# Kernel tuning notes

Measured on AMD Instinct MI355X. Metric: run time of the kernel, lower is better.

The kernel has to match this reference:

```python
import jax, jax.numpy as jnp
import numpy as np

# ---- config (matches init_kwargs) ----
M, N, D = 8, 512, 243            # meshes, neurons per mesh, input dim
E_RATIO = 0.8
NE = int(N * E_RATIO)            # 409 excitatory
NI = N - NE                      # 103 inhibitory
TICKS = 16
BATCH = 512
BITS = 4
WSCALE = 8.0
VTH, VRESET = 1.0, 0.0
TAU_E, TAU_I, DT = 2.0, 1.5, 1.0
BETA = 10.0                      # fast-sigmoid surrogate slope
INPUT_SCALE = 1.0


def fake_quant(w):
    """Quantization-aware fake quant with straight-through estimator."""
    step = WSCALE / (2 ** (BITS - 1))          # 1.0 for 4-bit, scale 8
    q = jnp.clip(jnp.round(w / step), -(2 ** (BITS - 1)), 2 ** (BITS - 1) - 1) * step
    return w + jax.lax.stop_gradient(q - w)


@jax.custom_vjp
def spike(u):
    return (u >= 0.0).astype(u.dtype)

def _spike_fwd(u):
    return spike(u), u

def _spike_bwd(u, g):
    # fast-sigmoid surrogate gradient
    return (g * BETA / (1.0 + BETA * jnp.abs(u)) ** 2,)

spike.defvjp(_spike_fwd, _spike_bwd)


def setup_inputs() -> dict:
    key = jax.random.key(0)
    ks = jax.random.split(key, 8)

    def sparse_w(k, shape, density, std, zero_diag=False):
        km, kw = jax.random.split(k)
        mask = (jax.random.uniform(km, shape) < density).astype(jnp.float32)
        if zero_diag:
            mask = mask * (1.0 - jnp.eye(shape[-1], dtype=jnp.float32))
        return jax.random.normal(kw, shape) * std * mask

    x = jax.random.normal(ks[0], (BATCH, D), dtype=jnp.float32)
    W_in = jax.random.normal(ks[1], (M, N, D)) * 0.8      # per-mesh input projection [out,in]
    b_in = jax.random.normal(ks[2], (M, N)) * 0.05
    W_inter = sparse_w(ks[3], (M, N, NE), 0.3, 0.8)        # inter-mesh: E of mesh m -> mesh m+1
    W_EE = sparse_w(ks[4], (M, NE, NE), 0.5, 0.8, True)
    W_EI = sparse_w(ks[5], (M, NI, NE), 0.6, 0.8)
    W_IE = sparse_w(ks[6], (M, NE, NI), 0.8, 0.8)
    W_II = sparse_w(ks[7], (M, NI, NI), 0.7, 0.8, True)
    return dict(x=x, W_in=W_in, b_in=b_in, W_inter=W_inter,
                W_EE=W_EE, W_EI=W_EI, W_IE=W_IE, W_II=W_II)


def reference(x, W_in, b_in, W_inter, W_EE, W_EI, W_IE, W_II):
    B = x.shape[0]
    decay_E = 1.0 - DT / TAU_E
    decay_I = 1.0 - DT / TAU_I

    # quantize weights once (constant across ticks)
    qW_in, qW_inter = fake_quant(W_in), fake_quant(W_inter)
    qW_EE, qW_EI = fake_quant(W_EE), fake_quant(W_EI)
    qW_IE, qW_II = fake_quant(W_IE), fake_quant(W_II)

    # external input projection, same every tick: [M, B, N]
    ext_proj = jnp.einsum('bd,mnd->mbn', x * INPUT_SCALE, qW_in) + b_in[:, None, :]

    def tick(carry, _):
        e, i, vE, vI, acc = carry          # e:[M,B,NE] i:[M,B,NI]
        # inter-mesh: mesh m receives inter_connections[m-1](e_prev[m-1])
        inter = jnp.einsum('mbe,mne->mbn', e, qW_inter)
        ext = ext_proj + jnp.roll(inter, 1, axis=0)
        cE = ext[:, :, :NE] \
            + jnp.einsum('mbe,mfe->mbf', e, qW_EE) \
            + jnp.einsum('mbi,mfi->mbf', i, qW_IE)
        cI = ext[:, :, NE:] \
            + jnp.einsum('mbe,mfe->mbf', e, qW_EI) \
            + jnp.einsum('mbi,mfi->mbf', i, qW_II)
        # LIF: leaky decay + input, threshold, hard reset
        vE = vE * decay_E + cE * DT
        vI = vI * decay_I + cI * DT
        sE = spike(vE - VTH)
        sI = spike(vI - VTH)
        vE = sE * VRESET + (1.0 - sE) * vE
        vI = sI * VRESET + (1.0 - sI) * vI
        acc = acc + jnp.concatenate([sE, sI], axis=-1)
        return (sE, sI, vE, vI, acc), None

    z = jnp.zeros
    carry0 = (z((M, B, NE)), z((M, B, NI)), z((M, B, NE)), z((M, B, NI)), z((M, B, N)))
    (eF, iF, vEF, vIF, acc), _ = jax.lax.scan(tick, carry0, None, length=TICKS)
    # accumulator laid out mesh-major: [B, M*N]
    return jnp.transpose(acc, (1, 0, 2)).reshape(B, M * N)
```

## Files before the change

kernel.cpp:

```cpp
#include <hip/hip_runtime.h>
#include <hip/hip_bf16.h>

#define Mm 8
#define Nn 512
#define NEe 409
#define NIi 103
#define Bb 512
#define Dd 243
#define Tt 16
#define SPB 96
#define WCROW 1152
#define DEC_I 0.33333334f
#define NBLK 256
#define FLAGSTRIDE 16
#define FLAGINTS 8192
#define SPINMAX 1000000L
#define ABROW 176

typedef int v4i __attribute__((ext_vector_type(4)));

__device__ __forceinline__ float quantf(float w) {
    float q = rintf(w);
    return fminf(fmaxf(q, -8.0f), 7.0f);
}

__device__ __forceinline__ v4i unpack16(unsigned int dl, unsigned int dh, bool qhi, int qsh) {
    unsigned int d = qhi ? dh : dl;
    v4i r;
    r[0] = (int)((((d >> qsh) & 0xFu) * 0x00204081u) & 0x01010101u);
    r[1] = (int)((((d >> (qsh + 4)) & 0xFu) * 0x00204081u) & 0x01010101u);
    r[2] = (int)((((d >> (qsh + 8)) & 0xFu) * 0x00204081u) & 0x01010101u);
    r[3] = (int)((((d >> (qsh + 12)) & 0xFu) * 0x00204081u) & 0x01010101u);
    return r;
}

__global__ void k_pack(const float* __restrict__ Wint, const float* __restrict__ WEE,
                       const float* __restrict__ WEI, const float* __restrict__ WIE,
                       const float* __restrict__ WII, signed char* __restrict__ Wc,
                       int* __restrict__ flags) {
    if (blockIdx.x == 0) {
        for (int i = threadIdx.x; i < FLAGINTS; i += 256) flags[i] = 0;
    }
    int q = blockIdx.x * 256 + threadIdx.x;
    if (q >= (Mm * Nn * WCROW) / 4) return;
    int k0 = (q * 4) % WCROW;
    int n  = ((q * 4) / WCROW) & (Nn - 1);
    int m  = (q * 4) / (WCROW * Nn);
    char out4[4];
#pragma unroll
    for (int j = 0; j < 4; ++j) {
        int k = k0 + j;
        float w = 0.0f;
        if (k < 512) {
            if (k < NEe) w = Wint[((((m + 7) & 7) * Nn) + n) * NEe + k];
        } else if (k < 1024) {
            int jj = k - 512;
            if (jj < NEe) w = (n < NEe) ? WEE[((m * NEe) + n) * NEe + jj]
                                        : WEI[((m * NIi) + (n - NEe)) * NEe + jj];
        } else {
            int jj = k - 1049;
            if (jj >= 0 && jj < NIi) w = (n < NEe) ? WIE[((m * NEe) + n) * NIi + jj]
                                        : WII[((m * NIi) + (n - NEe)) * NIi + jj];
        }
        out4[j] = (signed char)(int)quantf(w);
    }
    *(int*)&Wc[q * 4] = *(int*)out4;
}

__global__ void k_ext(const float* __restrict__ x, const float* __restrict__ Win,
                      const float* __restrict__ bin, float* __restrict__ ext) {
    __shared__ float xs[64][68];
    __shared__ float wsm[64][68];
    const int bid = blockIdx.x;
    const int m  = bid >> 6;
    const int bt = (bid >> 3) & 7;
    const int nt = bid & 7;
    const int b0 = bt * 64, n0 = nt * 64;
    const int t = threadIdx.x;
    const int tb4 = (t & 15) * 4;
    const int tn4 = (t >> 4) * 4;
    const int sr = t >> 2;
    const int sc = (t & 3) * 16;
    float c[4][4];
#pragma unroll
    for (int i = 0; i < 4; ++i)
#pragma unroll
        for (int j = 0; j < 4; ++j) c[i][j] = 0.0f;

    for (int d0 = 0; d0 < Dd; d0 += 64) {
#pragma unroll
        for (int j = 0; j < 16; ++j) {
            int d = d0 + sc + j;
            float xv = 0.0f, wv = 0.0f;
            if (d < Dd) {
                xv = x[(b0 + sr) * Dd + d];
                wv = quantf(Win[((m * Nn) + n0 + sr) * Dd + d]);
            }
            xs[sc + j][sr] = xv;
            wsm[sc + j][sr] = wv;
        }
        __syncthreads();
        const int dmax = min(64, Dd - d0);
        for (int d = 0; d < dmax; ++d) {
            float4 av = *(const float4*)&xs[d][tb4];
            float4 wv = *(const float4*)&wsm[d][tn4];
            float a[4] = {av.x, av.y, av.z, av.w};
            float wq[4] = {wv.x, wv.y, wv.z, wv.w};
#pragma unroll
            for (int i = 0; i < 4; ++i)
#pragma unroll
                for (int j = 0; j < 4; ++j)
                    c[i][j] = fmaf(a[i], wq[j], c[i][j]);
        }
        __syncthreads();
    }
#pragma unroll
    for (int i = 0; i < 4; ++i)
#pragma unroll
        for (int j = 0; j < 4; ++j) {
            float val = __fadd_rn(c[i][j], bin[m * Nn + n0 + tn4 + j]);
            ext[(size_t)(m * Bb + b0 + tb4 + i) * Nn + n0 + tn4 + j] = val;
        }
}

__global__ void __launch_bounds__(512, 2)
k_ticks(const signed char* __restrict__ Wc,
        unsigned char* __restrict__ Sp0,
        unsigned char* __restrict__ Sp1,
        const float* __restrict__ ext,
        float* __restrict__ out,
        int* __restrict__ flags) {
    __shared__ __align__(16) signed char sB[128 * WCROW];
    __shared__ __align__(16) unsigned char sAb[64 * ABROW];

    const int wg = blockIdx.x;
    const int m  = wg & 7;
    const int bt = (wg >> 3) & 7;
    const int nt = wg >> 6;
    const int b0 = bt * 64;
    const int n0 = nt * 128;
    const int pm = (m + 7) & 7;
    const int nm = (m + 1) & 7;

    const int tid  = threadIdx.x;
    const int w    = tid >> 6;
    const int lane = tid & 63;
    const int bh   = w & 1;
    const int nh   = w >> 1;
    const int quad = lane >> 4;
    const int li   = lane & 15;

    int waitIdx = 0;
    if (tid < 12) {
        int g  = tid >> 2;
        int mm = (g == 0) ? pm : ((g == 1) ? m : nm);
        waitIdx = (((tid & 3) << 6) | (bt << 3) | mm) * FLAGSTRIDE;
    }

    const signed char* WcBase = Wc + (size_t)(m * Nn + n0) * WCROW;
#pragma unroll
    for (int j = 0; j < 18; ++j) {
        int task = tid + j * 512;
        int row = task / 72, gg = task % 72;
        v4i v = *(const v4i*)(WcBase + (size_t)row * WCROW + gg * 16);
        int gs = (gg < 64) ? ((gg & 48) | ((gg ^ row) & 15))
                           : (64 + ((gg ^ row) & 7));
        *(v4i*)&sB[row * WCROW + gs * 16] = v;
    }

    float decs[2]; int nels[2];
    int styp[2], soff[2];
#pragma unroll
    for (int tn = 0; tn < 2; ++tn) {
        int n = n0 + nh * 32 + tn * 16 + li;
        nels[tn] = n;
        decs[tn] = (n < NEe) ? 0.5f : DEC_I;
        int nb = n0 + nh * 32 + tn * 16;
        if (nb < 400)      { styp[tn] = 0; soff[tn] = nb >> 3; }
        else if (nb == 400){ styp[tn] = 2; soff[tn] = 50; }
        else               { styp[tn] = 1; soff[tn] = 64 + ((nb - 384) >> 3); }
    }
    const int bbase = b0 + bh * 32;

    float extr[2][2][4];
#pragma unroll
    for (int tb = 0; tb < 2; ++tb)
#pragma unroll
        for (int tn = 0; tn < 2; ++tn)
#pragma unroll
            for (int r = 0; r < 4; ++r) {
                int b = bbase + tb * 16 + quad * 4 + r;
                extr[tb][tn][r] = ext[(size_t)(m * Bb + b) * Nn + nels[tn]];
            }
    float vmem[2][2][4];
    int cnt[2][2];
#pragma unroll
    for (int tb = 0; tb < 2; ++tb)
#pragma unroll
        for (int tn = 0; tn < 2; ++tn) {
            cnt[tb][tn] = 0;
#pragma unroll
            for (int r = 0; r < 4; ++r) vmem[tb][tn][r] = 0.0f;
        }

    if (nt == 0 && tid < 128) {
        int buf = tid >> 6, rr = tid & 63;
        unsigned char* base = (buf ? Sp1 : Sp0) + (size_t)(m * Bb + b0 + rr) * SPB;
        __hip_atomic_store((unsigned int*)(base + 52), 0u, __ATOMIC_RELAXED, __HIP_MEMORY_SCOPE_AGENT);
        __hip_atomic_store((unsigned int*)(base + 56), 0u, __ATOMIC_RELAXED, __HIP_MEMORY_SCOPE_AGENT);
        __hip_atomic_store((unsigned int*)(base + 60), 0u, __ATOMIC_RELAXED, __HIP_MEMORY_SCOPE_AGENT);
        __hip_atomic_store((unsigned short*)(base + 64), (unsigned short)0, __ATOMIC_RELAXED, __HIP_MEMORY_SCOPE_AGENT);
    }

    const bool qhi = (quad >= 2);
    const int qsh = (quad & 1) << 4;
    const int r0base = (bh * 32 + li) * ABROW;
    const int r1base = (bh * 32 + 16 + li) * ABROW;

    for (int t = 0; t < Tt; ++t) {
        unsigned char* SR = (t & 1) ? Sp1 : Sp0;
        unsigned char* SW = (t & 1) ? Sp0 : Sp1;

        if (t > 0) {
            if (tid < 12) {
                long spin = 0;
                while (__hip_atomic_load(&flags[waitIdx],
                                         __ATOMIC_RELAXED, __HIP_MEMORY_SCOPE_AGENT) < t) {
                    __builtin_amdgcn_s_sleep(2);
                    if (++spin > SPINMAX) break;
                }
            }
            __syncthreads();
        }

        float c[2][2][4];

        if (t == 0) {
#pragma unroll
            for (int tb = 0; tb < 2; ++tb)
#pragma unroll
                for (int tn = 0; tn < 2; ++tn)
#pragma unroll
                    for (int r = 0; r < 4; ++r)
                        c[tb][tn][r] = __fadd_rn(__fadd_rn(__fadd_rn(extr[tb][tn][r], 0.0f), 0.0f), 0.0f);
        } else {
            const unsigned char* PrevRow = SR + (size_t)(pm * Bb + b0) * SPB;
            const unsigned char* OwnRow  = SR + (size_t)(m  * Bb + b0) * SPB;
#pragma unroll
            for (int j = 0; j < 3; ++j) {
                int task = tid + j * 512;
                if (task < 1152) {
                    int row = task / 18, s = task % 18;
                    const unsigned char* src;
                    int dstoff;
                    if (s < 8)       { src = PrevRow + (size_t)row * SPB + s * 8;            dstoff = s * 8; }
                    else if (s < 16) { src = OwnRow  + (size_t)row * SPB + (s - 8) * 8;      dstoff = s * 8; }
                    else             { src = OwnRow  + (size_t)row * SPB + 64 + (s - 16) * 8; dstoff = 128 + (s - 16) * 8; }
                    unsigned long long vb = __hip_atomic_load((const unsigned long long*)src,
                                               __ATOMIC_RELAXED, __HIP_MEMORY_SCOPE_AGENT);
                    *(unsigned long long*)&sAb[row * ABROW + dstoff] = vb;
                }
            }
            __syncthreads();

            v4i acc[2][2];
#pragma unroll
            for (int tb = 0; tb < 2; ++tb)
#pragma unroll
                for (int tn = 0; tn < 2; ++tn) acc[tb][tn] = (v4i){0, 0, 0, 0};

#pragma unroll
            for (int ch = 0; ch < 4; ++ch) {
                const int cb = ch << 8;
                v4i a0lo = *(const v4i*)&sAb[r0base + (cb >> 3)];
                v4i a0hi = *(const v4i*)&sAb[r0base + (cb >> 3) + 16];
                v4i a1lo = *(const v4i*)&sAb[r1base + (cb >> 3)];
                v4i a1hi = *(const v4i*)&sAb[r1base + (cb >> 3) + 16];
#pragma unroll
                for (int ks = 0; ks < 256; ks += 64) {
                    v4i s0 = (ks < 128) ? a0lo : a0hi;
                    v4i s1 = (ks < 128) ? a1lo : a1hi;
                    const int D0 = ((ks >> 6) & 1) ? 2 : 0;
                    v4i af0 = unpack16((unsigned int)s0[D0], (unsigned int)s0[D0 + 1], qhi, qsh);
                    v4i af1 = unpack16((unsigned int)s1[D0], (unsigned int)s1[D0 + 1], qhi, qsh);
                    const int gs = (cb >> 4) + ((((ks >> 4) + quad) ^ li) & 15);
#pragma unroll
                    for (int tn = 0; tn < 2; ++tn) {
                        const v4i bfr = *(const v4i*)&sB[(nh * 32 + tn * 16 + li) * WCROW + gs * 16];
                        acc[0][tn] = __builtin_amdgcn_mfma_i32_16x16x64_i8(af0, bfr, acc[0][tn], 0, 0, 0);
                        acc[1][tn] = __builtin_amdgcn_mfma_i32_16x16x64_i8(af1, bfr, acc[1][tn], 0, 0, 0);
                    }
                }
                if (ch == 1) {
#pragma unroll
                    for (int tb = 0; tb < 2; ++tb)
#pragma unroll
                        for (int tn = 0; tn < 2; ++tn) {
#pragma unroll
                            for (int r = 0; r < 4; ++r)
                                c[tb][tn][r] = __fadd_rn(extr[tb][tn][r], (float)acc[tb][tn][r]);
                            acc[tb][tn] = (v4i){0, 0, 0, 0};
                        }
                } else if (ch == 3) {
#pragma unroll
                    for (int tb = 0; tb < 2; ++tb)
#pragma unroll
                        for (int tn = 0; tn < 2; ++tn) {
#pragma unroll
                            for (int r = 0; r < 4; ++r)
                                c[tb][tn][r] = __fadd_rn(c[tb][tn][r], (float)acc[tb][tn][r]);
                            acc[tb][tn] = (v4i){0, 0, 0, 0};
                        }
                }
            }
            {
                v4i e0 = *(const v4i*)&sAb[r0base + 128];
                v4i e1 = *(const v4i*)&sAb[r1base + 128];
#pragma unroll
                for (int ks = 0; ks < 128; ks += 64) {
                    const int D0 = (ks >> 6) ? 2 : 0;
                    v4i af0 = unpack16((unsigned int)e0[D0], (unsigned int)e0[D0 + 1], qhi, qsh);
                    v4i af1 = unpack16((unsigned int)e1[D0], (unsigned int)e1[D0 + 1], qhi, qsh);
                    const int gs = 64 + ((((ks >> 4) + quad) ^ li) & 7);
#pragma unroll
                    for (int tn = 0; tn < 2; ++tn) {
                        const v4i bfr = *(const v4i*)&sB[(nh * 32 + tn * 16 + li) * WCROW + gs * 16];
                        acc[0][tn] = __builtin_amdgcn_mfma_i32_16x16x64_i8(af0, bfr, acc[0][tn], 0, 0, 0);
                        acc[1][tn] = __builtin_amdgcn_mfma_i32_16x16x64_i8(af1, bfr, acc[1][tn], 0, 0, 0);
                    }
                }
            }
#pragma unroll
            for (int tb = 0; tb < 2; ++tb)
#pragma unroll
                for (int tn = 0; tn < 2; ++tn)
#pragma unroll
                    for (int r = 0; r < 4; ++r)
                        c[tb][tn][r] = __fadd_rn(c[tb][tn][r], (float)acc[tb][tn][r]);
        }

        int snow[2][2] = {{0, 0}, {0, 0}};
#pragma unroll
        for (int tb = 0; tb < 2; ++tb)
#pragma unroll
            for (int tn = 0; tn < 2; ++tn)
#pragma unroll
                for (int r = 0; r < 4; ++r) {
                    float vn = __fadd_rn(__fmul_rn(vmem[tb][tn][r], decs[tn]), c[tb][tn][r]);
                    int s = (vn >= 1.0f) ? 1 : 0;
                    vmem[tb][tn][r] = s ? 0.0f : vn;
                    cnt[tb][tn] += s << (r * 8);
                    snow[tb][tn] |= s << r;
                }

        if (t < Tt - 1) {
#pragma unroll
            for (int tb = 0; tb < 2; ++tb)
#pragma unroll
                for (int tn = 0; tn < 2; ++tn)
#pragma unroll
                    for (int r = 0; r < 4; ++r) {
                        unsigned long long mk = __ballot((snow[tb][tn] >> r) & 1);
                        if (li == 0) {
                            unsigned short v = (unsigned short)(mk >> (unsigned)(quad << 4));
                            int row = bbase + tb * 16 + quad * 4 + r;
                            unsigned char* rb = SW + (size_t)(m * Bb + row) * SPB;
                            if (styp[tn] != 2) {
                                __hip_atomic_store((unsigned short*)(rb + soff[tn]), v,
                                                   __ATOMIC_RELAXED, __HIP_MEMORY_SCOPE_AGENT);
                            } else {
                                __hip_atomic_store((unsigned short*)(rb + 50),
                                                   (unsigned short)(v & 0x01FF),
                                                   __ATOMIC_RELAXED, __HIP_MEMORY_SCOPE_AGENT);
                                __hip_atomic_store((unsigned short*)(rb + 66),
                                                   (unsigned short)(v & 0xFE00),
                                                   __ATOMIC_RELAXED, __HIP_MEMORY_SCOPE_AGENT);
                            }
                        }
                    }
        }

        if (t < Tt - 1) {
            __syncthreads();
            if (tid == 0)
                __hip_atomic_store(&flags[wg * FLAGSTRIDE], t + 1,
                                   __ATOMIC_RELAXED, __HIP_MEMORY_SCOPE_AGENT);
        }
    }

#pragma unroll
    for (int tb = 0; tb < 2; ++tb)
#pragma unroll
        for (int tn = 0; tn < 2; ++tn)
#pragma unroll
            for (int r = 0; r < 4; ++r) {
                int b = bbase + tb * 16 + quad * 4 + r;
                out[(size_t)b * (Mm * Nn) + m * Nn + nels[tn]] =
                    (float)((cnt[tb][tn] >> (r * 8)) & 0xff);
            }
}

extern "C" void kernel_launch(void* const* d_in, const int* in_sizes, int n_in,
                              void* d_out, int out_size, void* d_ws, size_t ws_size,
                              hipStream_t stream) {
    const float* x    = (const float*)d_in[0];
    const float* Win  = (const float*)d_in[1];
    const float* bin  = (const float*)d_in[2];
    const float* Wint = (const float*)d_in[3];
    const float* WEE  = (const float*)d_in[4];
    const float* WEI  = (const float*)d_in[5];
    const float* WIE  = (const float*)d_in[6];
    const float* WII  = (const float*)d_in[7];
    float* out = (float*)d_out;

    char* ws = (char*)d_ws;
    signed char* Wc    = (signed char*)ws;
    unsigned char* Sp0 = (unsigned char*)(ws + 4718592);
    unsigned char* Sp1 = Sp0 + 2621440;
    int* flags = (int*)(ws + 4718592 + 2 * 2621440);
    float* extw = (float*)(ws + 4718592 + 2 * 2621440 + 32768);

    k_pack<<<(Mm * Nn * WCROW / 4 + 255) / 256, 256, 0, stream>>>(Wint, WEE, WEI, WIE, WII, Wc, flags);
    k_ext<<<512, 256, 0, stream>>>(x, Win, bin, extw);
    k_ticks<<<NBLK, 512, 0, stream>>>(Wc, Sp0, Sp1, (const float*)extw, out, flags);
}
```

Before: 203.4 us.

## Replace per-tick flag waits with tagged spike words polled by consumers

Each spike bitmask word now carries the producing tick number in its upper 16 bits, so a consumer spins directly on the data it needs rather than waiting on per-workgroup flags before reading. The flag wait is kept only as a write-after-read guard before a block overwrites the double buffer, and it covers own-mesh and next-mesh readers instead of three meshes. The spike buffer rows double in size to hold the tags. The buffers are now zeroed in the pack kernel and the padding slots in shared memory are cleared once up front. This aims to cut barrier latency on the tick critical path, at the cost of more polling loads and larger stored rows.

```diff
diff --git a/kernel.cpp b/kernel.cpp
--- a/kernel.cpp
+++ b/kernel.cpp
@@ -8,7 +8,7 @@
 #define Bb 512
 #define Dd 243
 #define Tt 16
-#define SPB 96
+#define SPB 192
 #define WCROW 1152
 #define DEC_I 0.33333334f
 #define NBLK 256
@@ -16,6 +16,7 @@
 #define FLAGINTS 8192
 #define SPINMAX 1000000L
 #define ABROW 176
+#define SPZERO_U32 393216
 
 typedef int v4i __attribute__((ext_vector_type(4)));
 
@@ -37,11 +38,13 @@
 __global__ void k_pack(const float* __restrict__ Wint, const float* __restrict__ WEE,
                        const float* __restrict__ WEI, const float* __restrict__ WIE,
                        const float* __restrict__ WII, signed char* __restrict__ Wc,
-                       int* __restrict__ flags) {
+                       int* __restrict__ flags, unsigned* __restrict__ spz) {
+    int gid = blockIdx.x * 256 + threadIdx.x;
+    if (gid < SPZERO_U32) spz[gid] = 0u;
     if (blockIdx.x == 0) {
         for (int i = threadIdx.x; i < FLAGINTS; i += 256) flags[i] = 0;
     }
-    int q = blockIdx.x * 256 + threadIdx.x;
+    int q = gid;
     if (q >= (Mm * Nn * WCROW) / 4) return;
     int k0 = (q * 4) % WCROW;
     int n  = ((q * 4) / WCROW) & (Nn - 1);
@@ -150,11 +153,10 @@
     const int quad = lane >> 4;
     const int li   = lane & 15;
 
-    int waitIdx = 0;
-    if (tid < 12) {
-        int g  = tid >> 2;
-        int mm = (g == 0) ? pm : ((g == 1) ? m : nm);
-        waitIdx = (((tid & 3) << 6) | (bt << 3) | mm) * FLAGSTRIDE;
+    int warIdx = 0;
+    if (tid < 8) {
+        int mm = (tid < 4) ? m : nm;
+        warIdx = (((tid & 3) << 6) | (bt << 3) | mm) * FLAGSTRIDE;
     }
 
     const signed char* WcBase = Wc + (size_t)(m * Nn + n0) * WCROW;
@@ -168,17 +170,24 @@
         *(v4i*)&sB[row * WCROW + gs * 16] = v;
     }
 
+    if (tid < 384) {
+        int row = tid / 6, z = tid - (tid / 6) * 6;
+        int s = (z < 3) ? (13 + z) : (26 + z);
+        *(unsigned*)&sAb[row * ABROW + s * 4] = 0u;
+    }
+    __syncthreads();
+
     float decs[2]; int nels[2];
-    int styp[2], soff[2];
+    int sidxE[2], sidxI[2];
 #pragma unroll
     for (int tn = 0; tn < 2; ++tn) {
         int n = n0 + nh * 32 + tn * 16 + li;
         nels[tn] = n;
         decs[tn] = (n < NEe) ? 0.5f : DEC_I;
         int nb = n0 + nh * 32 + tn * 16;
-        if (nb < 400)      { styp[tn] = 0; soff[tn] = nb >> 3; }
-        else if (nb == 400){ styp[tn] = 2; soff[tn] = 50; }
-        else               { styp[tn] = 1; soff[tn] = 64 + ((nb - 384) >> 3); }
+        if (nb < 400)      { sidxE[tn] = nb >> 4;  sidxI[tn] = -1; }
+        else if (nb == 400){ sidxE[tn] = 25;       sidxI[tn] = 33; }
+        else               { sidxE[tn] = -1;       sidxI[tn] = 32 + ((nb - 384) >> 4); }
     }
     const int bbase = b0 + bh * 32;
 
@@ -202,15 +211,6 @@
 #pragma unroll
             for (int r = 0; r < 4; ++r) vmem[tb][tn][r] = 0.0f;
         }
-
-    if (nt == 0 && tid < 128) {
-        int buf = tid >> 6, rr = tid & 63;
-        unsigned char* base = (buf ? Sp1 : Sp0) + (size_t)(m * Bb + b0 + rr) * SPB;
-        __hip_atomic_store((unsigned int*)(base + 52), 0u, __ATOMIC_RELAXED, __HIP_MEMORY_SCOPE_AGENT);
-        __hip_atomic_store((unsigned int*)(base + 56), 0u, __ATOMIC_RELAXED, __HIP_MEMORY_SCOPE_AGENT);
-        __hip_atomic_store((unsigned int*)(base + 60), 0u, __ATOMIC_RELAXED, __HIP_MEMORY_SCOPE_AGENT);
-        __hip_atomic_store((unsigned short*)(base + 64), (unsigned short)0, __ATOMIC_RELAXED, __HIP_MEMORY_SCOPE_AGENT);
-    }
 
     const bool qhi = (quad >= 2);
     const int qsh = (quad & 1) << 4;
@@ -221,18 +221,6 @@
         unsigned char* SR = (t & 1) ? Sp1 : Sp0;
         unsigned char* SW = (t & 1) ? Sp0 : Sp1;
 
-        if (t > 0) {
-            if (tid < 12) {
-                long spin = 0;
-                while (__hip_atomic_load(&flags[waitIdx],
-                                         __ATOMIC_RELAXED, __HIP_MEMORY_SCOPE_AGENT) < t) {
-                    __builtin_amdgcn_s_sleep(2);
-                    if (++spin > SPINMAX) break;
-                }
-            }
-            __syncthreads();
-        }
-
         float c[2][2][4];
 
         if (t == 0) {
@@ -244,21 +232,43 @@
                     for (int r = 0; r < 4; ++r)
                         c[tb][tn][r] = __fadd_rn(__fadd_rn(__fadd_rn(extr[tb][tn][r], 0.0f), 0.0f), 0.0f);
         } else {
-            const unsigned char* PrevRow = SR + (size_t)(pm * Bb + b0) * SPB;
-            const unsigned char* OwnRow  = SR + (size_t)(m  * Bb + b0) * SPB;
-#pragma unroll
-            for (int j = 0; j < 3; ++j) {
+            const unsigned tg = (unsigned)t;
+#pragma unroll
+            for (int j = 0; j < 4; ++j) {
                 int task = tid + j * 512;
-                if (task < 1152) {
-                    int row = task / 18, s = task % 18;
-                    const unsigned char* src;
-                    int dstoff;
-                    if (s < 8)       { src = PrevRow + (size_t)row * SPB + s * 8;            dstoff = s * 8; }
-                    else if (s < 16) { src = OwnRow  + (size_t)row * SPB + (s - 8) * 8;      dstoff = s * 8; }
-                    else             { src = OwnRow  + (size_t)row * SPB + 64 + (s - 16) * 8; dstoff = 128 + (s - 16) * 8; }
-                    unsigned long long vb = __hip_atomic_load((const unsigned long long*)src,
-                                               __ATOMIC_RELAXED, __HIP_MEMORY_SCOPE_AGENT);
-                    *(unsigned long long*)&sAb[row * ABROW + dstoff] = vb;
+                if (task < 1920) {
+                    int row = task / 30;
+                    int sidx = task - row * 30;
+                    const unsigned long long* Pr = (const unsigned long long*)(SR + (size_t)(pm * Bb + b0 + row) * SPB);
+                    const unsigned long long* Ow = (const unsigned long long*)(SR + (size_t)(m  * Bb + b0 + row) * SPB);
+                    const unsigned long long* rp;
+                    int s; bool pair = true;
+                    if (sidx < 13)       { rp = Pr + sidx;          s = sidx; }
+                    else if (sidx < 26)  { rp = Ow + (sidx - 13);   s = 16 + (sidx - 13); }
+                    else if (sidx == 26) { rp = Ow + 16;            s = 32; pair = false; }
+                    else                 { int jj = sidx - 26; rp = Ow + 16 + jj; s = 32 + jj; }
+                    unsigned val;
+                    if (pair) {
+                        unsigned long long v = __hip_atomic_load(rp, __ATOMIC_RELAXED, __HIP_MEMORY_SCOPE_AGENT);
+                        long spin = 0;
+                        while ((((unsigned)v) >> 16) != tg || (((unsigned)(v >> 32)) >> 16) != tg) {
+                            __builtin_amdgcn_s_sleep(1);
+                            v = __hip_atomic_load(rp, __ATOMIC_RELAXED, __HIP_MEMORY_SCOPE_AGENT);
+                            if (++spin > SPINMAX) break;
+                        }
+                        val = ((unsigned)v & 0xFFFFu) | (((unsigned)(v >> 32)) << 16);
+                    } else {
+                        const unsigned* rp32 = (const unsigned*)rp + 1;
+                        unsigned v = __hip_atomic_load(rp32, __ATOMIC_RELAXED, __HIP_MEMORY_SCOPE_AGENT);
+                        long spin = 0;
+                        while ((v >> 16) != tg) {
+                            __builtin_amdgcn_s_sleep(1);
+                            v = __hip_atomic_load(rp32, __ATOMIC_RELAXED, __HIP_MEMORY_SCOPE_AGENT);
+                            if (++spin > SPINMAX) break;
+                        }
+                        val = v << 16;
+                    }
+                    *(unsigned*)&sAb[row * ABROW + s * 4] = val;
                 }
             }
             __syncthreads();
@@ -354,6 +364,16 @@
                 }
 
         if (t < Tt - 1) {
+            if (tid < 8) {
+                long spin = 0;
+                while (__hip_atomic_load(&flags[warIdx],
+                                         __ATOMIC_RELAXED, __HIP_MEMORY_SCOPE_AGENT) < t) {
+                    __builtin_amdgcn_s_sleep(2);
+                    if (++spin > SPINMAX) break;
+                }
+            }
+            __syncthreads();
+            const unsigned tagw = ((unsigned)(t + 1)) << 16;
 #pragma unroll
             for (int tb = 0; tb < 2; ++tb)
 #pragma unroll
@@ -362,25 +382,18 @@
                     for (int r = 0; r < 4; ++r) {
                         unsigned long long mk = __ballot((snow[tb][tn] >> r) & 1);
                         if (li == 0) {
-                            unsigned short v = (unsigned short)(mk >> (unsigned)(quad << 4));
+                            unsigned v16 = (unsigned)(unsigned short)(mk >> (unsigned)(quad << 4));
+                            unsigned wv = tagw | v16;
                             int row = bbase + tb * 16 + quad * 4 + r;
-                            unsigned char* rb = SW + (size_t)(m * Bb + row) * SPB;
-                            if (styp[tn] != 2) {
-                                __hip_atomic_store((unsigned short*)(rb + soff[tn]), v,
+                            unsigned* rb = (unsigned*)(SW + (size_t)(m * Bb + row) * SPB);
+                            if (sidxE[tn] >= 0)
+                                __hip_atomic_store(rb + sidxE[tn], wv,
                                                    __ATOMIC_RELAXED, __HIP_MEMORY_SCOPE_AGENT);
-                            } else {
-                                __hip_atomic_store((unsigned short*)(rb + 50),
-                                                   (unsigned short)(v & 0x01FF),
+                            if (sidxI[tn] >= 0)
+                                __hip_atomic_store(rb + sidxI[tn], wv,
                                                    __ATOMIC_RELAXED, __HIP_MEMORY_SCOPE_AGENT);
-                                __hip_atomic_store((unsigned short*)(rb + 66),
-                                                   (unsigned short)(v & 0xFE00),
-                                                   __ATOMIC_RELAXED, __HIP_MEMORY_SCOPE_AGENT);
-                            }
                         }
                     }
-        }
-
-        if (t < Tt - 1) {
             __syncthreads();
             if (tid == 0)
                 __hip_atomic_store(&flags[wg * FLAGSTRIDE], t + 1,
@@ -416,11 +429,12 @@
     char* ws = (char*)d_ws;
     signed char* Wc    = (signed char*)ws;
     unsigned char* Sp0 = (unsigned char*)(ws + 4718592);
-    unsigned char* Sp1 = Sp0 + 2621440;
-    int* flags = (int*)(ws + 4718592 + 2 * 2621440);
-    float* extw = (float*)(ws + 4718592 + 2 * 2621440 + 32768);
-
-    k_pack<<<(Mm * Nn * WCROW / 4 + 255) / 256, 256, 0, stream>>>(Wint, WEE, WEI, WIE, WII, Wc, flags);
+    unsigned char* Sp1 = Sp0 + 786432;
+    int* flags = (int*)(ws + 4718592 + 1572864);
+    float* extw = (float*)(ws + 4718592 + 1572864 + 32768);
+
+    k_pack<<<(Mm * Nn * WCROW / 4 + 255) / 256, 256, 0, stream>>>(Wint, WEE, WEI, WIE, WII, Wc,
+                                                                  flags, (unsigned*)Sp0);
     k_ext<<<512, 256, 0, stream>>>(x, Win, bin, extw);
     k_ticks<<<NBLK, 512, 0, stream>>>(Wc, Sp0, Sp1, (const float*)extw, out, flags);
 }
```

Result: slower. 234.1 us (+15.1%).

## Fuse input projection into tick kernel and use per-tick spike buffers

Applied to the files above, without the earlier changes.

Removes the separate ext-projection kernel by computing each block's 64x128 slice of the input projection in shared memory at the start of the tick kernel. Replaces the double-buffered spike arrays with one buffer per tick, which are zeroed (together with the flags) in the pack kernel. Each block now waits only on the previous and own mesh flags, no longer on the next mesh, since write-after-read hazards disappear. The cost is more workspace zeroing in the pack kernel and a larger prologue in the tick kernel.

```diff
diff --git a/kernel.cpp b/kernel.cpp
--- a/kernel.cpp
+++ b/kernel.cpp
@@ -9,13 +9,14 @@
 #define Dd 243
 #define Tt 16
 #define SPB 96
+#define SPTICK (Mm * Bb * SPB)
 #define WCROW 1152
 #define DEC_I 0.33333334f
 #define NBLK 256
 #define FLAGSTRIDE 16
-#define FLAGINTS 8192
 #define SPINMAX 1000000L
 #define ABROW 176
+#define ZSPAN_U32 1581056
 
 typedef int v4i __attribute__((ext_vector_type(4)));
 
@@ -37,11 +38,14 @@
 __global__ void k_pack(const float* __restrict__ Wint, const float* __restrict__ WEE,
                        const float* __restrict__ WEI, const float* __restrict__ WIE,
                        const float* __restrict__ WII, signed char* __restrict__ Wc,
-                       int* __restrict__ flags) {
-    if (blockIdx.x == 0) {
-        for (int i = threadIdx.x; i < FLAGINTS; i += 256) flags[i] = 0;
-    }
-    int q = blockIdx.x * 256 + threadIdx.x;
+                       unsigned* __restrict__ spz) {
+    int gid = blockIdx.x * 256 + threadIdx.x;
+#pragma unroll
+    for (int z = 0; z < 2; ++z) {
+        int i = gid + z * 1179648;
+        if (i < ZSPAN_U32) spz[i] = 0u;
+    }
+    int q = gid;
     if (q >= (Mm * Nn * WCROW) / 4) return;
     int k0 = (q * 4) % WCROW;
     int n  = ((q * 4) / WCROW) & (Nn - 1);
@@ -67,67 +71,12 @@
     *(int*)&Wc[q * 4] = *(int*)out4;
 }
 
-__global__ void k_ext(const float* __restrict__ x, const float* __restrict__ Win,
-                      const float* __restrict__ bin, float* __restrict__ ext) {
-    __shared__ float xs[64][68];
-    __shared__ float wsm[64][68];
-    const int bid = blockIdx.x;
-    const int m  = bid >> 6;
-    const int bt = (bid >> 3) & 7;
-    const int nt = bid & 7;
-    const int b0 = bt * 64, n0 = nt * 64;
-    const int t = threadIdx.x;
-    const int tb4 = (t & 15) * 4;
-    const int tn4 = (t >> 4) * 4;
-    const int sr = t >> 2;
-    const int sc = (t & 3) * 16;
-    float c[4][4];
-#pragma unroll
-    for (int i = 0; i < 4; ++i)
-#pragma unroll
-        for (int j = 0; j < 4; ++j) c[i][j] = 0.0f;
-
-    for (int d0 = 0; d0 < Dd; d0 += 64) {
-#pragma unroll
-        for (int j = 0; j < 16; ++j) {
-            int d = d0 + sc + j;
-            float xv = 0.0f, wv = 0.0f;
-            if (d < Dd) {
-                xv = x[(b0 + sr) * Dd + d];
-                wv = quantf(Win[((m * Nn) + n0 + sr) * Dd + d]);
-            }
-            xs[sc + j][sr] = xv;
-            wsm[sc + j][sr] = wv;
-        }
-        __syncthreads();
-        const int dmax = min(64, Dd - d0);
-        for (int d = 0; d < dmax; ++d) {
-            float4 av = *(const float4*)&xs[d][tb4];
-            float4 wv = *(const float4*)&wsm[d][tn4];
-            float a[4] = {av.x, av.y, av.z, av.w};
-            float wq[4] = {wv.x, wv.y, wv.z, wv.w};
-#pragma unroll
-            for (int i = 0; i < 4; ++i)
-#pragma unroll
-                for (int j = 0; j < 4; ++j)
-                    c[i][j] = fmaf(a[i], wq[j], c[i][j]);
-        }
-        __syncthreads();
-    }
-#pragma unroll
-    for (int i = 0; i < 4; ++i)
-#pragma unroll
-        for (int j = 0; j < 4; ++j) {
-            float val = __fadd_rn(c[i][j], bin[m * Nn + n0 + tn4 + j]);
-            ext[(size_t)(m * Bb + b0 + tb4 + i) * Nn + n0 + tn4 + j] = val;
-        }
-}
-
 __global__ void __launch_bounds__(512, 2)
 k_ticks(const signed char* __restrict__ Wc,
-        unsigned char* __restrict__ Sp0,
-        unsigned char* __restrict__ Sp1,
-        const float* __restrict__ ext,
+        unsigned char* __restrict__ Sp,
+        const float* __restrict__ x,
+        const float* __restrict__ Win,
+        const float* __restrict__ bin,
         float* __restrict__ out,
         int* __restrict__ flags) {
     __shared__ __align__(16) signed char sB[128 * WCROW];
@@ -140,7 +89,6 @@
     const int b0 = bt * 64;
     const int n0 = nt * 128;
     const int pm = (m + 7) & 7;
-    const int nm = (m + 1) & 7;
 
     const int tid  = threadIdx.x;
     const int w    = tid >> 6;
@@ -151,21 +99,9 @@
     const int li   = lane & 15;
 
     int waitIdx = 0;
-    if (tid < 12) {
-        int g  = tid >> 2;
-        int mm = (g == 0) ? pm : ((g == 1) ? m : nm);
+    if (tid < 8) {
+        int mm = (tid < 4) ? pm : m;
         waitIdx = (((tid & 3) << 6) | (bt << 3) | mm) * FLAGSTRIDE;
-    }
-
-    const signed char* WcBase = Wc + (size_t)(m * Nn + n0) * WCROW;
-#pragma unroll
-    for (int j = 0; j < 18; ++j) {
-        int task = tid + j * 512;
-        int row = task / 72, gg = task % 72;
-        v4i v = *(const v4i*)(WcBase + (size_t)row * WCROW + gg * 16);
-        int gs = (gg < 64) ? ((gg & 48) | ((gg ^ row) & 15))
-                           : (64 + ((gg ^ row) & 7));
-        *(v4i*)&sB[row * WCROW + gs * 16] = v;
     }
 
     float decs[2]; int nels[2];
@@ -182,16 +118,87 @@
     }
     const int bbase = b0 + bh * 32;
 
+    {
+        const int g   = tid >> 8;
+        const int t8  = tid & 255;
+        const int n0e = n0 + g * 64;
+        float* xs  = (float*)sB + g * (2 * 64 * 68);
+        float* wsm = xs + 64 * 68;
+        const int etb4 = (t8 & 15) * 4;
+        const int etn4 = (t8 >> 4) * 4;
+        const int sr = t8 >> 2;
+        const int sc = (t8 & 3) * 16;
+        float c[4][4];
+#pragma unroll
+        for (int i = 0; i < 4; ++i)
+#pragma unroll
+            for (int j = 0; j < 4; ++j) c[i][j] = 0.0f;
+
+        for (int d0 = 0; d0 < Dd; d0 += 64) {
+#pragma unroll
+            for (int j = 0; j < 16; ++j) {
+                int d = d0 + sc + j;
+                float xv = 0.0f, wv = 0.0f;
+                if (d < Dd) {
+                    xv = x[(b0 + sr) * Dd + d];
+                    wv = quantf(Win[((m * Nn) + n0e + sr) * Dd + d]);
+                }
+                xs[(sc + j) * 68 + sr] = xv;
+                wsm[(sc + j) * 68 + sr] = wv;
+            }
+            __syncthreads();
+            const int dmax = min(64, Dd - d0);
+            for (int d = 0; d < dmax; ++d) {
+                float4 av = *(const float4*)&xs[d * 68 + etb4];
+                float4 wv = *(const float4*)&wsm[d * 68 + etn4];
+                float a[4] = {av.x, av.y, av.z, av.w};
+                float wq[4] = {wv.x, wv.y, wv.z, wv.w};
+#pragma unroll
+                for (int i = 0; i < 4; ++i)
+#pragma unroll
+                    for (int j = 0; j < 4; ++j)
+                        c[i][j] = fmaf(a[i], wq[j], c[i][j]);
+            }
+            __syncthreads();
+        }
+        float* extbuf = (float*)sB;
+#pragma unroll
+        for (int i = 0; i < 4; ++i)
+#pragma unroll
+            for (int j = 0; j < 4; ++j)
+                extbuf[(etb4 + i) * 128 + g * 64 + etn4 + j] =
+                    __fadd_rn(c[i][j], bin[m * Nn + n0e + etn4 + j]);
+        __syncthreads();
+    }
+
     float extr[2][2][4];
 #pragma unroll
     for (int tb = 0; tb < 2; ++tb)
 #pragma unroll
         for (int tn = 0; tn < 2; ++tn)
 #pragma unroll
-            for (int r = 0; r < 4; ++r) {
-                int b = bbase + tb * 16 + quad * 4 + r;
-                extr[tb][tn][r] = ext[(size_t)(m * Bb + b) * Nn + nels[tn]];
-            }
+            for (int r = 0; r < 4; ++r)
+                extr[tb][tn][r] = ((const float*)sB)[(bh * 32 + tb * 16 + quad * 4 + r) * 128
+                                                     + (nels[tn] - n0)];
+    __syncthreads();
+
+    const signed char* WcBase = Wc + (size_t)(m * Nn + n0) * WCROW;
+#pragma unroll
+    for (int j = 0; j < 18; ++j) {
+        int task = tid + j * 512;
+        int row = task / 72, gg = task % 72;
+        v4i v = *(const v4i*)(WcBase + (size_t)row * WCROW + gg * 16);
+        int gs = (gg < 64) ? ((gg & 48) | ((gg ^ row) & 15))
+                           : (64 + ((gg ^ row) & 7));
+        *(v4i*)&sB[row * WCROW + gs * 16] = v;
+    }
+    if (tid < 384) {
+        int row = tid / 6, z = tid - (tid / 6) * 6;
+        int s = (z < 3) ? (13 + z) : (26 + z);
+        *(unsigned*)&sAb[row * ABROW + s * 4] = 0u;
+    }
+    __syncthreads();
+
     float vmem[2][2][4];
     int cnt[2][2];
 #pragma unroll
@@ -202,15 +209,6 @@
 #pragma unroll
             for (int r = 0; r < 4; ++r) vmem[tb][tn][r] = 0.0f;
         }
-
-    if (nt == 0 && tid < 128) {
-        int buf = tid >> 6, rr = tid & 63;
-        unsigned char* base = (buf ? Sp1 : Sp0) + (size_t)(m * Bb + b0 + rr) * SPB;
-        __hip_atomic_store((unsigned int*)(base + 52), 0u, __ATOMIC_RELAXED, __HIP_MEMORY_SCOPE_AGENT);
-        __hip_atomic_store((unsigned int*)(base + 56), 0u, __ATOMIC_RELAXED, __HIP_MEMORY_SCOPE_AGENT);
-        __hip_atomic_store((unsigned int*)(base + 60), 0u, __ATOMIC_RELAXED, __HIP_MEMORY_SCOPE_AGENT);
-        __hip_atomic_store((unsigned short*)(base + 64), (unsigned short)0, __ATOMIC_RELAXED, __HIP_MEMORY_SCOPE_AGENT);
-    }
 
     const bool qhi = (quad >= 2);
     const int qsh = (quad & 1) << 4;
@@ -218,11 +216,18 @@
     const int r1base = (bh * 32 + 16 + li) * ABROW;
 
     for (int t = 0; t < Tt; ++t) {
-        unsigned char* SR = (t & 1) ? Sp1 : Sp0;
-        unsigned char* SW = (t & 1) ? Sp0 : Sp1;
-
-        if (t > 0) {
-            if (tid < 12) {
+        float c[2][2][4];
+
+        if (t == 0) {
+#pragma unroll
+            for (int tb = 0; tb < 2; ++tb)
+#pragma unroll
+                for (int tn = 0; tn < 2; ++tn)
+#pragma unroll
+                    for (int r = 0; r < 4; ++r)
+                        c[tb][tn][r] = __fadd_rn(__fadd_rn(__fadd_rn(extr[tb][tn][r], 0.0f), 0.0f), 0.0f);
+        } else {
+            if (tid < 8) {
                 long spin = 0;
                 while (__hip_atomic_load(&flags[waitIdx],
                                          __ATOMIC_RELAXED, __HIP_MEMORY_SCOPE_AGENT) < t) {
@@ -231,19 +236,8 @@
                 }
             }
             __syncthreads();
-        }
-
-        float c[2][2][4];
-
-        if (t == 0) {
-#pragma unroll
-            for (int tb = 0; tb < 2; ++tb)
-#pragma unroll
-                for (int tn = 0; tn < 2; ++tn)
-#pragma unroll
-                    for (int r = 0; r < 4; ++r)
-                        c[tb][tn][r] = __fadd_rn(__fadd_rn(__fadd_rn(extr[tb][tn][r], 0.0f), 0.0f), 0.0f);
-        } else {
+
+            const unsigned char* SR = Sp + (size_t)(t - 1) * SPTICK;
             const unsigned char* PrevRow = SR + (size_t)(pm * Bb + b0) * SPB;
             const unsigned char* OwnRow  = SR + (size_t)(m  * Bb + b0) * SPB;
 #pragma unroll
@@ -354,6 +348,7 @@
                 }
 
         if (t < Tt - 1) {
+            unsigned char* SW = Sp + (size_t)t * SPTICK;
 #pragma unroll
             for (int tb = 0; tb < 2; ++tb)
 #pragma unroll
@@ -378,9 +373,6 @@
                             }
                         }
                     }
-        }
-
-        if (t < Tt - 1) {
             __syncthreads();
             if (tid == 0)
                 __hip_atomic_store(&flags[wg * FLAGSTRIDE], t + 1,
@@ -414,13 +406,11 @@
     float* out = (float*)d_out;
 
     char* ws = (char*)d_ws;
-    signed char* Wc    = (signed char*)ws;
-    unsigned char* Sp0 = (unsigned char*)(ws + 4718592);
-    unsigned char* Sp1 = Sp0 + 2621440;
-    int* flags = (int*)(ws + 4718592 + 2 * 2621440);
-    float* extw = (float*)(ws + 4718592 + 2 * 2621440 + 32768);
-
-    k_pack<<<(Mm * Nn * WCROW / 4 + 255) / 256, 256, 0, stream>>>(Wint, WEE, WEI, WIE, WII, Wc, flags);
-    k_ext<<<512, 256, 0, stream>>>(x, Win, bin, extw);
-    k_ticks<<<NBLK, 512, 0, stream>>>(Wc, Sp0, Sp1, (const float*)extw, out, flags);
+    signed char* Wc   = (signed char*)ws;
+    unsigned char* Sp = (unsigned char*)(ws + 4718592);
+    int* flags = (int*)(ws + 4718592 + 16 * SPTICK);
+
+    k_pack<<<(Mm * Nn * WCROW / 4 + 255) / 256, 256, 0, stream>>>(Wint, WEE, WEI, WIE, WII, Wc,
+                                                                  (unsigned*)Sp);
+    k_ticks<<<NBLK, 512, 0, stream>>>(Wc, Sp, x, Win, bin, out, flags);
 }
```

Result: faster. 197.0 us (median of 3 runs) (-3.2%).
